# Kernel optimization log

Hardware: AMD Instinct MI355X
Metric: run time of the kernel (lower is better)

The kernel has to match this reference:

```python
import jax, jax.numpy as jnp
import numpy as np

W_MAX = 256  # max words per sentence (word ids 1..W_MAX; 0 = special/pad subwords)


def setup_inputs() -> dict:
    key = jax.random.key(0)
    k1, k2 = jax.random.split(key)
    L, B, S, F = 4, 32, 512, 768
    hidden_states = jax.random.normal(k1, (L, B, S, F), dtype=jnp.float32)
    layer_weights = jnp.ones((L,), dtype=jnp.float32)
    gamma = jnp.ones((1,), dtype=jnp.float32)
    # contiguous ragged word spans: sorted word ids per subword position
    word_ids = jnp.sort(
        jax.random.randint(k2, (B, S), 0, W_MAX + 1, dtype=jnp.int32), axis=1
    )
    return {
        "hidden_states": hidden_states,
        "layer_weights": layer_weights,
        "gamma": gamma,
        "word_ids": word_ids,
    }


def reference(hidden_states, layer_weights, gamma, word_ids):
    L, B, S, F = hidden_states.shape
    num_seg = B * (W_MAX + 1)

    # weighted layer mixing (weight_layers=True branch)
    normal_weights = jax.nn.softmax(layer_weights)
    subword_embeddings = gamma * jnp.einsum("l,lbsf->bsf", normal_weights, hidden_states)

    # fused segment-mean over ragged word spans
    flat = subword_embeddings.reshape(B * S, F)
    seg = (word_ids + jnp.arange(B, dtype=word_ids.dtype)[:, None] * (W_MAX + 1)).reshape(-1)
    sums = jax.ops.segment_sum(flat, seg, num_segments=num_seg)
    counts = jax.ops.segment_sum(
        jnp.ones((B * S,), dtype=flat.dtype), seg, num_segments=num_seg
    )
    means = sums / jnp.maximum(counts, 1.0)[:, None]  # empty words stay zero

    word_embeddings = means.reshape(B, W_MAX + 1, F)
    # slot 0: mean over all subword positions (sentence embedding)
    word_embeddings = word_embeddings.at[:, 0, :].set(subword_embeddings.mean(axis=1))
    return word_embeddings
```

## Files before the change

### kernel.cpp

```cpp
#include <hip/hip_runtime.h>

#define LL 4
#define BB 32
#define SS 512
#define FF 768
#define NW 257
#define F4 192

typedef float f4v __attribute__((ext_vector_type(4)));

__global__ __launch_bounds__(256, 3)
void k_main(const float* __restrict__ hs, const float* __restrict__ lw,
            const float* __restrict__ gm, const int* __restrict__ wid,
            float* __restrict__ out, float* __restrict__ partials) {
    int bid = blockIdx.x;
    int fc = bid % 3;
    int sg = (bid / 3) & 7;
    int b  = bid / 24;
    int t = threadIdx.x;
    int lane = t & 63;
    int swave = t >> 6;
    int f4 = fc * 64 + lane;
    int s0 = sg * 64 + swave * 16;

    float w0 = lw[0], w1 = lw[1], w2 = lw[2], w3 = lw[3];
    float mx = fmaxf(fmaxf(w0, w1), fmaxf(w2, w3));
    float e0 = __expf(w0 - mx), e1 = __expf(w1 - mx);
    float e2 = __expf(w2 - mx), e3 = __expf(w3 - mx);
    float g = gm[0] / (e0 + e1 + e2 + e3);
    float c0 = e0 * g, c1 = e1 * g, c2 = e2 * g, c3 = e3 * g;

    const f4v* h4 = (const f4v*)hs;
    const int ls = BB * SS * F4;
    int base = (b * SS + s0) * F4 + f4;
    const int* wrow = wid + b * SS + s0;

    int prev = wrow[0];
    bool sharedL = (s0 > 0) && (wrow[-1] == prev);
    bool sharedR = (s0 + 16 < SS) && (wrow[16] == wrow[15]);

    f4v sent = {0.f, 0.f, 0.f, 0.f};
    f4v run  = {0.f, 0.f, 0.f, 0.f};
    int len = 0;
    bool first = true;

    #pragma unroll
    for (int k = 0; k < 16; k++) {
        int w = wrow[k];
        int idx = base + k * F4;
        f4v a  = __builtin_nontemporal_load(&h4[idx]);
        f4v bv = __builtin_nontemporal_load(&h4[idx + ls]);
        f4v cv = __builtin_nontemporal_load(&h4[idx + 2 * ls]);
        f4v dv = __builtin_nontemporal_load(&h4[idx + 3 * ls]);
        f4v v = c0 * a + c1 * bv + c2 * cv + c3 * dv;
        sent += v;
        if (w != prev) {
            float* p = out + (prev + b * NW) * FF + f4 * 4;
            if (first && sharedL) {
                atomicAdd(p + 0, run.x); atomicAdd(p + 1, run.y);
                atomicAdd(p + 2, run.z); atomicAdd(p + 3, run.w);
            } else {
                *(f4v*)p = run * (1.0f / (float)len);
            }
            first = false;
            run = v; len = 1; prev = w;
        } else {
            run += v; len++;
        }
    }
    {
        float* p = out + (prev + b * NW) * FF + f4 * 4;
        if ((first && sharedL) || sharedR) {
            atomicAdd(p + 0, run.x); atomicAdd(p + 1, run.y);
            atomicAdd(p + 2, run.z); atomicAdd(p + 3, run.w);
        } else {
            *(f4v*)p = run * (1.0f / (float)len);
        }
    }

    __shared__ f4v sm[256];
    sm[t] = sent;
    __syncthreads();
    if (t < 64) {
        f4v tot = sm[t] + sm[t + 64] + sm[t + 128] + sm[t + 192];
        ((f4v*)partials)[(b * 8 + sg) * F4 + f4] = tot;
    }
}

__global__ void k_fix(const int* __restrict__ wid,
                      const float* __restrict__ partials,
                      float* __restrict__ out) {
    __shared__ int lc[NW];
    __shared__ int flag[NW];
    int b = blockIdx.x;
    int t = threadIdx.x;
    for (int i = t; i < NW; i += 512) { lc[i] = 0; flag[i] = 0; }
    __syncthreads();
    int w = wid[b * SS + t];
    atomicAdd(&lc[w], 1);
    if (t > 0 && (t & 15) == 0) {
        if (wid[b * SS + t - 1] == w) flag[w] = 1;
    }
    __syncthreads();
    for (int w2 = 1; w2 < NW; ++w2) {
        if (flag[w2]) {
            float inv = 1.0f / (float)(lc[w2] > 1 ? lc[w2] : 1);
            float* p = out + ((size_t)b * NW + w2) * FF;
            for (int f = t; f < FF; f += 512) p[f] *= inv;
        }
    }
    const float* pp = partials + (size_t)b * 8 * FF;
    for (int f = t; f < FF; f += 512) {
        float s = 0.f;
        #pragma unroll
        for (int gg = 0; gg < 8; gg++) s += pp[gg * FF + f];
        out[(size_t)b * NW * FF + f] = s * (1.0f / (float)SS);
    }
}

extern "C" void kernel_launch(void* const* d_in, const int* in_sizes, int n_in,
                              void* d_out, int out_size, void* d_ws, size_t ws_size,
                              hipStream_t stream) {
    const float* hs  = (const float*)d_in[0];
    const float* lw  = (const float*)d_in[1];
    const float* gm  = (const float*)d_in[2];
    const int*   wid = (const int*)d_in[3];
    float* out = (float*)d_out;

    float* partials = (float*)d_ws;

    (void)hipMemsetAsync(d_out, 0, (size_t)out_size * sizeof(float), stream);
    k_main<<<BB * 24, 256, 0, stream>>>(hs, lw, gm, wid, out, partials);
    k_fix<<<BB, 512, 0, stream>>>(wid, partials, out);
}
```

Baseline: 309.0 us.

## Route boundary-word atomics to small scratch and drop full output memset

Words that span 16-position window boundaries now have their partial sums atomically added into a small per-window scratch buffer instead of the output. The fix kernel combines these per word and also writes zeros for empty words. This lets the full-output memset shrink to a memset of the scratch buffer only, cutting the extra write pass over the output. The cost is more work in the single-block-per-batch fix kernel, which now loops over all words and scans the window slots for each.

After: 324.3 us. 1.05x slower.

```diff
diff --git a/kernel.cpp b/kernel.cpp
--- a/kernel.cpp
+++ b/kernel.cpp
@@ -6,13 +6,15 @@
 #define FF 768
 #define NW 257
 #define F4 192
+#define NSLOT 32
 
 typedef float f4v __attribute__((ext_vector_type(4)));
 
 __global__ __launch_bounds__(256, 3)
 void k_main(const float* __restrict__ hs, const float* __restrict__ lw,
             const float* __restrict__ gm, const int* __restrict__ wid,
-            float* __restrict__ out, float* __restrict__ partials) {
+            float* __restrict__ out, float* __restrict__ bsum,
+            float* __restrict__ partials) {
     int bid = blockIdx.x;
     int fc = bid % 3;
     int sg = (bid / 3) & 7;
@@ -22,6 +24,7 @@
     int swave = t >> 6;
     int f4 = fc * 64 + lane;
     int s0 = sg * 64 + swave * 16;
+    int win = s0 >> 4;
 
     float w0 = lw[0], w1 = lw[1], w2 = lw[2], w3 = lw[3];
     float mx = fmaxf(fmaxf(w0, w1), fmaxf(w2, w3));
@@ -55,11 +58,12 @@
         f4v v = c0 * a + c1 * bv + c2 * cv + c3 * dv;
         sent += v;
         if (w != prev) {
-            float* p = out + (prev + b * NW) * FF + f4 * 4;
             if (first && sharedL) {
+                float* p = bsum + ((size_t)(b * NSLOT + win) * FF) + f4 * 4;
                 atomicAdd(p + 0, run.x); atomicAdd(p + 1, run.y);
                 atomicAdd(p + 2, run.z); atomicAdd(p + 3, run.w);
             } else {
+                float* p = out + (prev + b * NW) * FF + f4 * 4;
                 *(f4v*)p = run * (1.0f / (float)len);
             }
             first = false;
@@ -69,11 +73,16 @@
         }
     }
     {
-        float* p = out + (prev + b * NW) * FF + f4 * 4;
-        if ((first && sharedL) || sharedR) {
+        if (first && sharedL) {
+            float* p = bsum + ((size_t)(b * NSLOT + win) * FF) + f4 * 4;
+            atomicAdd(p + 0, run.x); atomicAdd(p + 1, run.y);
+            atomicAdd(p + 2, run.z); atomicAdd(p + 3, run.w);
+        } else if (sharedR) {
+            float* p = bsum + ((size_t)(b * NSLOT + win + 1) * FF) + f4 * 4;
             atomicAdd(p + 0, run.x); atomicAdd(p + 1, run.y);
             atomicAdd(p + 2, run.z); atomicAdd(p + 3, run.w);
         } else {
+            float* p = out + (prev + b * NW) * FF + f4 * 4;
             *(f4v*)p = run * (1.0f / (float)len);
         }
     }
@@ -88,33 +97,62 @@
 }
 
 __global__ void k_fix(const int* __restrict__ wid,
+                      const float* __restrict__ bsum,
                       const float* __restrict__ partials,
                       float* __restrict__ out) {
+    __shared__ int wrow[SS];
     __shared__ int lc[NW];
-    __shared__ int flag[NW];
+    __shared__ int bw[NSLOT];
     int b = blockIdx.x;
     int t = threadIdx.x;
-    for (int i = t; i < NW; i += 512) { lc[i] = 0; flag[i] = 0; }
+    for (int i = t; i < NW; i += 512) lc[i] = 0;
     __syncthreads();
     int w = wid[b * SS + t];
+    wrow[t] = w;
     atomicAdd(&lc[w], 1);
-    if (t > 0 && (t & 15) == 0) {
-        if (wid[b * SS + t - 1] == w) flag[w] = 1;
-    }
     __syncthreads();
-    for (int w2 = 1; w2 < NW; ++w2) {
-        if (flag[w2]) {
-            float inv = 1.0f / (float)(lc[w2] > 1 ? lc[w2] : 1);
-            float* p = out + ((size_t)b * NW + w2) * FF;
-            for (int f = t; f < FF; f += 512) p[f] *= inv;
+    if (t < NSLOT)
+        bw[t] = (t >= 1 && wrow[16 * t - 1] == wrow[16 * t]) ? wrow[16 * t] : -1;
+    __syncthreads();
+
+    int wave = t >> 6;
+    int lane = t & 63;
+    const f4v* bs4 = (const f4v*)(bsum + (size_t)b * NSLOT * FF);
+    for (int w2 = 1 + wave; w2 < NW; w2 += 8) {
+        int c = lc[w2];
+        f4v* po = (f4v*)(out + ((size_t)b * NW + w2) * FF);
+        if (c == 0) {
+            f4v z = {0.f, 0.f, 0.f, 0.f};
+            #pragma unroll
+            for (int i = 0; i < 3; i++) po[lane + 64 * i] = z;
+        } else {
+            bool has = false;
+            f4v acc0 = {0.f,0.f,0.f,0.f}, acc1 = acc0, acc2 = acc0;
+            for (int k = 1; k < NSLOT; k++) {
+                if (bw[k] == w2) {
+                    has = true;
+                    const f4v* pb = bs4 + (size_t)k * F4;
+                    acc0 += pb[lane];
+                    acc1 += pb[lane + 64];
+                    acc2 += pb[lane + 128];
+                }
+            }
+            if (has) {
+                float inv = 1.0f / (float)c;
+                po[lane]       = acc0 * inv;
+                po[lane + 64]  = acc1 * inv;
+                po[lane + 128] = acc2 * inv;
+            }
         }
     }
-    const float* pp = partials + (size_t)b * 8 * FF;
-    for (int f = t; f < FF; f += 512) {
-        float s = 0.f;
+
+    __syncthreads();
+    if (t < F4) {
+        const f4v* pp = (const f4v*)(partials + (size_t)b * 8 * FF);
+        f4v s = {0.f, 0.f, 0.f, 0.f};
         #pragma unroll
-        for (int gg = 0; gg < 8; gg++) s += pp[gg * FF + f];
-        out[(size_t)b * NW * FF + f] = s * (1.0f / (float)SS);
+        for (int gg = 0; gg < 8; gg++) s += pp[(size_t)gg * F4 + t];
+        ((f4v*)(out + (size_t)b * NW * FF))[t] = s * (1.0f / (float)SS);
     }
 }
 
@@ -127,9 +165,10 @@
     const int*   wid = (const int*)d_in[3];
     float* out = (float*)d_out;
 
-    float* partials = (float*)d_ws;
+    float* bsum     = (float*)d_ws;
+    float* partials = bsum + (size_t)BB * NSLOT * FF;
 
-    (void)hipMemsetAsync(d_out, 0, (size_t)out_size * sizeof(float), stream);
-    k_main<<<BB * 24, 256, 0, stream>>>(hs, lw, gm, wid, out, partials);
-    k_fix<<<BB, 512, 0, stream>>>(wid, partials, out);
+    (void)hipMemsetAsync(bsum, 0, (size_t)BB * NSLOT * FF * sizeof(float), stream);
+    k_main<<<BB * 24, 256, 0, stream>>>(hs, lw, gm, wid, out, bsum, partials);
+    k_fix<<<BB, 512, 0, stream>>>(wid, bsum, partials, out);
 }
```

## Replace atomics and memset with per-window edge partials and parallel fixup

Applied to the files above, without the earlier changes.

The main kernel now uses 8-subword windows and launches twice as many blocks with higher occupancy. Each window records its leftmost and rightmost partial word sums in a workspace buffer, which replaces the global atomicAdd path. The fixup kernel is spread over 8 chunks per batch. For each word it binary-searches the span, combines the boundary partials for words that cross windows, and writes zeros for empty words, so the output memset is dropped. The cost is extra workspace traffic and a heavier fixup pass.

Measured after the change: 289.8 us, median of 2. 1.07x faster.

```diff
diff --git a/kernel.cpp b/kernel.cpp
--- a/kernel.cpp
+++ b/kernel.cpp
@@ -1,27 +1,30 @@
 #include <hip/hip_runtime.h>
 
-#define LL 4
 #define BB 32
 #define SS 512
 #define FF 768
 #define NW 257
 #define F4 192
+#define WIN 8
+#define NWIN 64
 
 typedef float f4v __attribute__((ext_vector_type(4)));
 
-__global__ __launch_bounds__(256, 3)
+__global__ __launch_bounds__(256, 6)
 void k_main(const float* __restrict__ hs, const float* __restrict__ lw,
             const float* __restrict__ gm, const int* __restrict__ wid,
-            float* __restrict__ out, float* __restrict__ partials) {
+            float* __restrict__ out, float* __restrict__ lr,
+            float* __restrict__ partials) {
     int bid = blockIdx.x;
     int fc = bid % 3;
-    int sg = (bid / 3) & 7;
-    int b  = bid / 24;
+    int sg = (bid / 3) & 15;
+    int b  = bid / 48;
     int t = threadIdx.x;
     int lane = t & 63;
     int swave = t >> 6;
     int f4 = fc * 64 + lane;
-    int s0 = sg * 64 + swave * 16;
+    int s0 = sg * 32 + swave * 8;
+    int win = s0 >> 3;
 
     float w0 = lw[0], w1 = lw[1], w2 = lw[2], w3 = lw[3];
     float mx = fmaxf(fmaxf(w0, w1), fmaxf(w2, w3));
@@ -37,7 +40,10 @@
 
     int prev = wrow[0];
     bool sharedL = (s0 > 0) && (wrow[-1] == prev);
-    bool sharedR = (s0 + 16 < SS) && (wrow[16] == wrow[15]);
+    bool sharedR = (s0 + WIN < SS) && (wrow[WIN] == wrow[WIN - 1]);
+
+    f4v* lrw = (f4v*)lr + (size_t)(b * NWIN + win) * 2 * F4;
+    f4v* ob  = (f4v*)out + (size_t)b * NW * F4;
 
     f4v sent = {0.f, 0.f, 0.f, 0.f};
     f4v run  = {0.f, 0.f, 0.f, 0.f};
@@ -45,8 +51,7 @@
     bool first = true;
 
     #pragma unroll
-    for (int k = 0; k < 16; k++) {
-        int w = wrow[k];
+    for (int k = 0; k < WIN; k++) {
         int idx = base + k * F4;
         f4v a  = __builtin_nontemporal_load(&h4[idx]);
         f4v bv = __builtin_nontemporal_load(&h4[idx + ls]);
@@ -54,13 +59,14 @@
         f4v dv = __builtin_nontemporal_load(&h4[idx + 3 * ls]);
         f4v v = c0 * a + c1 * bv + c2 * cv + c3 * dv;
         sent += v;
-        if (w != prev) {
-            float* p = out + (prev + b * NW) * FF + f4 * 4;
-            if (first && sharedL) {
-                atomicAdd(p + 0, run.x); atomicAdd(p + 1, run.y);
-                atomicAdd(p + 2, run.z); atomicAdd(p + 3, run.w);
+        int w = wrow[k];
+        if (k > 0 && w != prev) {
+            if (first) {
+                lrw[f4] = run;
+                if (!sharedL)
+                    ob[(size_t)prev * F4 + f4] = run * (1.0f / (float)len);
             } else {
-                *(f4v*)p = run * (1.0f / (float)len);
+                ob[(size_t)prev * F4 + f4] = run * (1.0f / (float)len);
             }
             first = false;
             run = v; len = 1; prev = w;
@@ -69,12 +75,13 @@
         }
     }
     {
-        float* p = out + (prev + b * NW) * FF + f4 * 4;
-        if ((first && sharedL) || sharedR) {
-            atomicAdd(p + 0, run.x); atomicAdd(p + 1, run.y);
-            atomicAdd(p + 2, run.z); atomicAdd(p + 3, run.w);
-        } else {
-            *(f4v*)p = run * (1.0f / (float)len);
+        lrw[F4 + f4] = run;
+        if (first) {
+            lrw[f4] = run;
+            if (!sharedL && !sharedR)
+                ob[(size_t)prev * F4 + f4] = run * (1.0f / (float)len);
+        } else if (!sharedR) {
+            ob[(size_t)prev * F4 + f4] = run * (1.0f / (float)len);
         }
     }
 
@@ -83,38 +90,64 @@
     __syncthreads();
     if (t < 64) {
         f4v tot = sm[t] + sm[t + 64] + sm[t + 128] + sm[t + 192];
-        ((f4v*)partials)[(b * 8 + sg) * F4 + f4] = tot;
+        ((f4v*)partials)[((size_t)b * 16 + sg) * F4 + f4] = tot;
     }
 }
 
-__global__ void k_fix(const int* __restrict__ wid,
-                      const float* __restrict__ partials,
-                      float* __restrict__ out) {
-    __shared__ int lc[NW];
-    __shared__ int flag[NW];
-    int b = blockIdx.x;
+__global__ __launch_bounds__(256, 4)
+void k_fix(const int* __restrict__ wid,
+           const float* __restrict__ lr,
+           const float* __restrict__ partials,
+           float* __restrict__ out) {
+    __shared__ int ww[SS];
+    int bid = blockIdx.x;
+    int b = bid >> 3;
+    int chunk = bid & 7;
     int t = threadIdx.x;
-    for (int i = t; i < NW; i += 512) { lc[i] = 0; flag[i] = 0; }
+    ww[t]       = wid[b * SS + t];
+    ww[t + 256] = wid[b * SS + t + 256];
     __syncthreads();
-    int w = wid[b * SS + t];
-    atomicAdd(&lc[w], 1);
-    if (t > 0 && (t & 15) == 0) {
-        if (wid[b * SS + t - 1] == w) flag[w] = 1;
-    }
-    __syncthreads();
-    for (int w2 = 1; w2 < NW; ++w2) {
-        if (flag[w2]) {
-            float inv = 1.0f / (float)(lc[w2] > 1 ? lc[w2] : 1);
-            float* p = out + ((size_t)b * NW + w2) * FF;
-            for (int f = t; f < FF; f += 512) p[f] *= inv;
+
+    int wave = t >> 6, lane = t & 63;
+    const f4v* lr4 = (const f4v*)lr + (size_t)b * NWIN * 2 * F4;
+    f4v* ob = (f4v*)out + (size_t)b * NW * F4;
+
+    for (int i = wave; i < 32; i += 4) {
+        int w2 = 1 + chunk + 8 * i;
+        int lo = 0, hi = SS;
+        while (lo < hi) { int m = (lo + hi) >> 1; if (ww[m] < w2) lo = m + 1; else hi = m; }
+        int sa = lo;
+        lo = 0; hi = SS;
+        while (lo < hi) { int m = (lo + hi) >> 1; if (ww[m] < w2 + 1) lo = m + 1; else hi = m; }
+        int se = lo - 1;
+
+        f4v* po = ob + (size_t)w2 * F4;
+        if (sa > se) {
+            f4v z = {0.f, 0.f, 0.f, 0.f};
+            po[lane] = z; po[lane + 64] = z; po[lane + 128] = z;
+        } else {
+            int i0 = sa >> 3, j0 = se >> 3;
+            if (i0 != j0) {
+                f4v a0 = lr4[((size_t)i0 * 2 + 1) * F4 + lane];
+                f4v a1 = lr4[((size_t)i0 * 2 + 1) * F4 + lane + 64];
+                f4v a2 = lr4[((size_t)i0 * 2 + 1) * F4 + lane + 128];
+                for (int k = i0 + 1; k <= j0; k++) {
+                    a0 += lr4[((size_t)k * 2) * F4 + lane];
+                    a1 += lr4[((size_t)k * 2) * F4 + lane + 64];
+                    a2 += lr4[((size_t)k * 2) * F4 + lane + 128];
+                }
+                float inv = 1.0f / (float)(se - sa + 1);
+                po[lane] = a0 * inv; po[lane + 64] = a1 * inv; po[lane + 128] = a2 * inv;
+            }
         }
     }
-    const float* pp = partials + (size_t)b * 8 * FF;
-    for (int f = t; f < FF; f += 512) {
-        float s = 0.f;
+
+    if (chunk == 0 && t < F4) {
+        const f4v* pp = (const f4v*)partials + (size_t)b * 16 * F4;
+        f4v s = {0.f, 0.f, 0.f, 0.f};
         #pragma unroll
-        for (int gg = 0; gg < 8; gg++) s += pp[gg * FF + f];
-        out[(size_t)b * NW * FF + f] = s * (1.0f / (float)SS);
+        for (int g2 = 0; g2 < 16; g2++) s += pp[(size_t)g2 * F4 + t];
+        ob[t] = s * (1.0f / (float)SS);
     }
 }
 
@@ -127,9 +160,9 @@
     const int*   wid = (const int*)d_in[3];
     float* out = (float*)d_out;
 
-    float* partials = (float*)d_ws;
+    float* lr       = (float*)d_ws;
+    float* partials = lr + (size_t)BB * NWIN * 2 * FF;
 
-    (void)hipMemsetAsync(d_out, 0, (size_t)out_size * sizeof(float), stream);
-    k_main<<<BB * 24, 256, 0, stream>>>(hs, lw, gm, wid, out, partials);
-    k_fix<<<BB, 512, 0, stream>>>(wid, partials, out);
+    k_main<<<BB * 48, 256, 0, stream>>>(hs, lw, gm, wid, out, lr, partials);
+    k_fix<<<BB * 8, 256, 0, stream>>>(wid, lr, partials, out);
 }
```
